# Optimization experiments

Hardware: AMD Instinct MI355X
Metric: run time of the kernel (lower is better)

Reference implementation:

```python
import jax, jax.numpy as jnp
import numpy as np

DIM = 1024
HEADS = 16
DIM_HEAD = 64
INNER = HEADS * DIM_HEAD  # == DIM, so project_out Linear is shape-consistent
SCALE = DIM_HEAD ** -0.5
EPS = 1e-5


def setup_inputs() -> dict:
    key = jax.random.key(0)
    ks = jax.random.split(key, 8)
    std = 0.02
    return {
        "x": jax.random.normal(ks[0], (2, 2048, DIM), dtype=jnp.float32),
        "gamma": jnp.ones((DIM,), dtype=jnp.float32),
        "beta": jnp.zeros((DIM,), dtype=jnp.float32),
        "wq": jax.random.normal(ks[1], (DIM, INNER), dtype=jnp.float32) * std,
        "wk": jax.random.normal(ks[2], (DIM, INNER), dtype=jnp.float32) * std,
        "wv": jax.random.normal(ks[3], (DIM, INNER), dtype=jnp.float32) * std,
        "wo": jax.random.normal(ks[4], (INNER, DIM), dtype=jnp.float32) * std,
        "w_out": jax.random.normal(ks[5], (INNER, DIM), dtype=jnp.float32) * std,
        "b_out": jnp.zeros((DIM,), dtype=jnp.float32),
    }


def reference(x, gamma, beta, wq, wk, wv, wo, w_out, b_out):
    b, n, d = x.shape
    # LayerNorm
    mu = jnp.mean(x, axis=-1, keepdims=True)
    var = jnp.mean(jnp.square(x - mu), axis=-1, keepdims=True)
    xn = (x - mu) * jax.lax.rsqrt(var + EPS) * gamma + beta
    # QKV projections -> [b, h, n, dh]
    def split_heads(t):
        return t.reshape(b, n, HEADS, DIM_HEAD).transpose(0, 2, 1, 3)
    q = split_heads(xn @ wq)
    k = split_heads(xn @ wk)
    v = split_heads(xn @ wv)
    scores = jnp.einsum('bhqd,bhkd->bhqk', q, k) * SCALE
    attn = jax.nn.softmax(scores, axis=-1)
    out = jnp.einsum('bhqk,bhkd->bhqd', attn, v)
    out = out.transpose(0, 2, 1, 3).reshape(b, n, INNER)
    out = out @ wo               # wo: inner -> dim
    out = out @ w_out + b_out    # project_out Linear (dropout=0 -> identity)
    return out
```

## Files before the change

kernel.cpp:

```cpp
#include <hip/hip_runtime.h>

typedef _Float16 f16;
typedef _Float16 f16x2 __attribute__((ext_vector_type(2)));
typedef _Float16 f16x4 __attribute__((ext_vector_type(4)));
typedef _Float16 f16x8 __attribute__((ext_vector_type(8)));
typedef float f32x4 __attribute__((ext_vector_type(4)));

#define MFMA_F16(a, b, c) __builtin_amdgcn_mfma_f32_16x16x32_f16(a, b, c, 0, 0, 0)
#define ASYNC16(g, l) __builtin_amdgcn_global_load_lds(                              \
    (const __attribute__((address_space(1))) void*)(g),                              \
    (__attribute__((address_space(3))) void*)(l), 16, 0, 0)

__global__ __launch_bounds__(256)
void pre_kernel(const float* __restrict__ x, const float* __restrict__ gamma,
                const float* __restrict__ beta, f16* __restrict__ xn,
                const float* __restrict__ wq, const float* __restrict__ wk,
                const float* __restrict__ wv, const float* __restrict__ wo,
                const float* __restrict__ wout,
                f16* __restrict__ wqt, f16* __restrict__ wkt, f16* __restrict__ wvt,
                f16* __restrict__ wo_h, f16* __restrict__ woutt)
{
    const int t = threadIdx.x;
    if (blockIdx.x < 4096) {
        const int row = blockIdx.x;
        const float* xr = x + (size_t)row * 1024;
        float4 v = *(const float4*)(xr + t * 4);
        float s  = v.x + v.y + v.z + v.w;
        float ss = v.x * v.x + v.y * v.y + v.z * v.z + v.w * v.w;
#pragma unroll
        for (int off = 32; off > 0; off >>= 1) {
            s  += __shfl_down(s, off);
            ss += __shfl_down(ss, off);
        }
        __shared__ float wsum[4], wsq[4];
        const int wid = t >> 6, lane = t & 63;
        if (lane == 0) { wsum[wid] = s; wsq[wid] = ss; }
        __syncthreads();
        const float fs  = wsum[0] + wsum[1] + wsum[2] + wsum[3];
        const float fss = wsq[0] + wsq[1] + wsq[2] + wsq[3];
        const float mu  = fs * (1.0f / 1024.0f);
        const float var = fss * (1.0f / 1024.0f) - mu * mu;
        const float rs  = rsqrtf(var + 1e-5f);
        float4 g = *(const float4*)(gamma + t * 4);
        float4 b = *(const float4*)(beta + t * 4);
        f16x4 o;
        o[0] = (f16)((v.x - mu) * rs * g.x + b.x);
        o[1] = (f16)((v.y - mu) * rs * g.y + b.y);
        o[2] = (f16)((v.z - mu) * rs * g.z + b.z);
        o[3] = (f16)((v.w - mu) * rs * g.w + b.w);
        *(f16x4*)(xn + (size_t)row * 1024 + t * 4) = o;
        return;
    }
    const int pb = blockIdx.x - 4096;
    const int z = pb >> 8, rem = pb & 255;
    const int bx = rem & 15, by = rem >> 4;
    const float* src; f16* dst; int tr; float scl = 1.0f;
    switch (z) {
        case 0:  src = wq;   dst = wqt;   tr = 1; scl = 0.18033688011f; break;
        case 1:  src = wk;   dst = wkt;   tr = 1; break;
        case 2:  src = wv;   dst = wvt;   tr = 1; break;
        case 3:  src = wo;   dst = wo_h;  tr = 0; break;
        default: src = wout; dst = woutt; tr = 1; break;
    }
    const int r0 = by * 64, c0 = bx * 64;
    if (!tr) {
#pragma unroll
        for (int i = 0; i < 16; i++) {
            int idx = t + 256 * i;
            int r = idx >> 6, c = idx & 63;
            dst[(size_t)(r0 + r) * 1024 + c0 + c] = (f16)src[(size_t)(r0 + r) * 1024 + c0 + c];
        }
    } else {
        __shared__ __align__(16) f16 T[64][72];
#pragma unroll
        for (int i = 0; i < 16; i++) {
            int idx = t + 256 * i;
            int r = idx >> 6, c = idx & 63;
            T[r][c] = (f16)(src[(size_t)(r0 + r) * 1024 + c0 + c] * scl);
        }
        __syncthreads();
#pragma unroll
        for (int i = 0; i < 16; i++) {
            int idx = t + 256 * i;
            int r = idx >> 6, c = idx & 63;
            dst[(size_t)(c0 + r) * 1024 + r0 + c] = T[c][r];
        }
    }
}

__global__ __launch_bounds__(256, 3)
void gemm_qkv_w2(const f16* __restrict__ A, const f16* __restrict__ Bt,
                 f16* __restrict__ Qd, f16* __restrict__ Kd, f16* __restrict__ Vd,
                 const f16* __restrict__ A2, const f16* __restrict__ Bt2,
                 f16* __restrict__ W2t)
{
    __shared__ __align__(16) f16 smem[2 * 128 * 64];
    f16* As = smem;
    f16* Bs = smem + 128 * 64;
    const int tid = threadIdx.x;
    const int wid = tid >> 6, lane = tid & 63;
    const int qq = lane >> 4, ml = lane & 15;
    const int row0 = (wid >> 1) * 64, col0 = (wid & 1) * 64;

    int mode, bx, by;
    const f16 *Abase, *Bbase;
    if (blockIdx.y < 24) {
        mode = 0; bx = blockIdx.x; by = blockIdx.y; Abase = A; Bbase = Bt;
    } else {
        mode = 1;
        int id = (blockIdx.y - 24) * 32 + blockIdx.x;
        bx = id & 7; by = id >> 3; Abase = A2; Bbase = Bt2;
    }
    const f16* Ab = Abase + (size_t)bx * 128 * 1024;
    const f16* Bb = Bbase + (size_t)by * 128 * 1024;
    const int sr = lane >> 3;
    const int sc = ((lane & 7) ^ sr) * 8;
    const int swz = ml & 7;

    f32x4 acc[4][4];
#pragma unroll
    for (int i = 0; i < 4; i++)
#pragma unroll
        for (int j = 0; j < 4; j++) acc[i][j] = (f32x4){0.f, 0.f, 0.f, 0.f};

    for (int k0 = 0; k0 < 1024; k0 += 64) {
        __syncthreads();
#pragma unroll
        for (int j = 0; j < 4; j++) {
            const int inst = wid * 4 + j;
            const int r = inst * 8 + sr;
            ASYNC16(Ab + (size_t)r * 1024 + k0 + sc, &As[inst * 512]);
            ASYNC16(Bb + (size_t)r * 1024 + k0 + sc, &Bs[inst * 512]);
        }
        __syncthreads();
#pragma unroll
        for (int kh = 0; kh < 2; kh++) {
            f16x8 af[4], bf[4];
#pragma unroll
            for (int mb = 0; mb < 4; mb++)
                af[mb] = *(const f16x8*)(&As[(row0 + mb * 16 + ml) * 64 + ((kh * 4 + qq) ^ swz) * 8]);
#pragma unroll
            for (int nb = 0; nb < 4; nb++)
                bf[nb] = *(const f16x8*)(&Bs[(col0 + nb * 16 + ml) * 64 + ((kh * 4 + qq) ^ swz) * 8]);
#pragma unroll
            for (int mb = 0; mb < 4; mb++)
#pragma unroll
                for (int nb = 0; nb < 4; nb++)
                    acc[mb][nb] = MFMA_F16(af[mb], bf[nb], acc[mb][nb]);
        }
    }

    if (mode == 1) {
        const int rT = bx * 128 + row0 + qq * 4;
#pragma unroll
        for (int mb = 0; mb < 4; mb++)
#pragma unroll
            for (int nb = 0; nb < 4; nb++) {
                int c = by * 128 + col0 + nb * 16 + ml;
#pragma unroll
                for (int rg = 0; rg < 4; rg++)
                    W2t[(size_t)(rT + mb * 16 + rg) * 1024 + c] = (f16)acc[mb][nb][rg];
            }
        return;
    }
    __syncthreads();
    f16* Cs = smem;
    const int sel = (by * 128) >> 10;
    const int bb  = (bx * 128) >> 11;
    const int nl0 = (bx * 128) & 2047;
    const int h0  = (by & 7) * 2;
    if (sel < 2) {
#pragma unroll
        for (int mb = 0; mb < 4; mb++)
#pragma unroll
            for (int nb = 0; nb < 4; nb++) {
                int col = col0 + nb * 16 + ml;
#pragma unroll
                for (int rg = 0; rg < 4; rg++) {
                    int row = row0 + mb * 16 + qq * 4 + rg;
                    int ch = (col >> 3) ^ (row & 15);
                    Cs[row * 128 + ch * 8 + (col & 7)] = (f16)acc[mb][nb][rg];
                }
            }
        __syncthreads();
        f16* Dst = (sel == 0 ? Qd : Kd);
#pragma unroll
        for (int i = 0; i < 8; i++) {
            int idx = i * 256 + tid;
            int r = idx >> 4, ch = idx & 15;
            f16x8 v = *(const f16x8*)(&Cs[r * 128 + ((ch ^ (r & 15)) * 8)]);
            int hh = h0 + (ch >> 3), d0 = (ch & 7) * 8;
            *(f16x8*)(Dst + ((size_t)(bb * 16 + hh) * 2048 + nl0 + r) * 64 + d0) = v;
        }
    } else {
#pragma unroll
        for (int mb = 0; mb < 4; mb++)
#pragma unroll
            for (int nb = 0; nb < 4; nb++) {
                int col = col0 + nb * 16 + ml;
                int rch = ((row0 + mb * 16) >> 3) + (qq >> 1);
                int ch = rch ^ (col & 15);
                f16x4 w;
                w[0] = (f16)acc[mb][nb][0]; w[1] = (f16)acc[mb][nb][1];
                w[2] = (f16)acc[mb][nb][2]; w[3] = (f16)acc[mb][nb][3];
                *(f16x4*)(&Cs[col * 128 + ch * 8 + (qq & 1) * 4]) = w;
            }
        __syncthreads();
#pragma unroll
        for (int i = 0; i < 8; i++) {
            int idx = i * 256 + tid;
            int c = idx >> 4, tc = idx & 15;
            f16x8 v = *(const f16x8*)(&Cs[c * 128 + ((tc ^ (c & 15)) * 8)]);
            int hh = h0 + (c >> 6), d = c & 63;
            *(f16x8*)(Vd + ((size_t)(bb * 16 + hh) * 64 + d) * 2048 + nl0 + tc * 8) = v;
        }
    }
}

__global__ __launch_bounds__(256, 4)
void flash_kernel(const f16* __restrict__ Q, const f16* __restrict__ K,
                  const f16* __restrict__ Vt, f16* __restrict__ O)
{
    __shared__ __align__(16) f16 Ks[2][64 * 64];
    __shared__ __align__(16) f16 Vts[2][64 * 64];
    __shared__ __align__(16) f16 Ps[4][16 * 64];

    const int bh = blockIdx.y;
    const int q0 = blockIdx.x * 64;
    const int tid = threadIdx.x, wid = tid >> 6, lane = tid & 63;
    const int qq = lane >> 4, ml = lane & 15;

    const f16* Qb = Q + ((size_t)bh * 2048 + q0 + wid * 16) * 64;
    const f16* Kb = K + (size_t)bh * 2048 * 64;
    const f16* Vb = Vt + (size_t)bh * 64 * 2048;

    f16x8 qf[2];
#pragma unroll
    for (int kh = 0; kh < 2; kh++)
        qf[kh] = *(const f16x8*)(Qb + (size_t)ml * 64 + kh * 32 + qq * 8);

    f32x4 oacc[4];
    float lsum = 0.f;
#pragma unroll
    for (int nd = 0; nd < 4; nd++) oacc[nd] = (f32x4){0.f, 0.f, 0.f, 0.f};

    const int sr = lane >> 3, scw = ((lane & 7) ^ sr) * 8;
    const int swz = ml & 7;
    f16* Psw = Ps[wid];

#pragma unroll
    for (int j = 0; j < 2; j++) {
        const int inst = wid * 2 + j;
        const int r = inst * 8 + sr;
        ASYNC16(Kb + (size_t)r * 64 + scw, &Ks[0][inst * 512]);
        ASYNC16(Vb + (size_t)r * 2048 + 0 + scw, &Vts[0][inst * 512]);
    }
    __syncthreads();

    for (int t = 0; t < 32; t++) {
        const int buf = t & 1;
        if (t < 31) {
            const int t1 = (t + 1) * 64;
#pragma unroll
            for (int j = 0; j < 2; j++) {
                const int inst = wid * 2 + j;
                const int r = inst * 8 + sr;
                ASYNC16(Kb + ((size_t)t1 + r) * 64 + scw, &Ks[buf ^ 1][inst * 512]);
                ASYNC16(Vb + (size_t)r * 2048 + t1 + scw, &Vts[buf ^ 1][inst * 512]);
            }
        }

        f32x4 s[4];
#pragma unroll
        for (int nb = 0; nb < 4; nb++) s[nb] = (f32x4){0.f, 0.f, 0.f, 0.f};
#pragma unroll
        for (int nb = 0; nb < 4; nb++)
#pragma unroll
            for (int kh = 0; kh < 2; kh++) {
                f16x8 kb = *(const f16x8*)(&Ks[buf][(nb * 16 + ml) * 64 + ((kh * 4 + qq) ^ swz) * 8]);
                s[nb] = MFMA_F16(kb, qf[kh], s[nb]);
            }

#pragma unroll
        for (int nb = 0; nb < 4; nb++) {
            float p0 = __builtin_amdgcn_exp2f(s[nb][0]);
            float p1 = __builtin_amdgcn_exp2f(s[nb][1]);
            float p2 = __builtin_amdgcn_exp2f(s[nb][2]);
            float p3 = __builtin_amdgcn_exp2f(s[nb][3]);
            lsum += (p0 + p1) + (p2 + p3);
            f16x2 lo = __builtin_bit_cast(f16x2, __builtin_amdgcn_cvt_pkrtz(p0, p1));
            f16x2 hi = __builtin_bit_cast(f16x2, __builtin_amdgcn_cvt_pkrtz(p2, p3));
            f16x4 w = __builtin_shufflevector(lo, hi, 0, 1, 2, 3);
            int ch = (2 * nb + (qq >> 1)) ^ swz;
            *(f16x4*)(&Psw[ml * 64 + ch * 8 + (qq & 1) * 4]) = w;
        }

#pragma unroll
        for (int ks = 0; ks < 2; ks++) {
            f16x8 pa = *(const f16x8*)(&Psw[ml * 64 + ((ks * 4 + 2 * (qq >> 1) + (qq & 1)) ^ swz) * 8]);
#pragma unroll
            for (int nd = 0; nd < 4; nd++) {
                f16x8 vb = *(const f16x8*)(&Vts[buf][(nd * 16 + ml) * 64 + ((ks * 4 + qq) ^ swz) * 8]);
                oacc[nd] = MFMA_F16(pa, vb, oacc[nd]);
            }
        }
        __syncthreads();
    }

    lsum += __shfl_xor(lsum, 16);
    lsum += __shfl_xor(lsum, 32);

    const int bb = bh >> 4, hh = bh & 15;
#pragma unroll
    for (int r = 0; r < 4; r++) {
        float linv = 1.0f / __shfl(lsum, qq * 4 + r, 16);
        int tok = q0 + wid * 16 + qq * 4 + r;
        size_t base = ((size_t)(bb * 2048 + tok)) * 1024 + hh * 64;
#pragma unroll
        for (int nd = 0; nd < 4; nd++)
            O[base + nd * 16 + ml] = (f16)(oacc[nd][r] * linv);
    }
}

__global__ __launch_bounds__(256, 3)
void gemm_final(const f16* __restrict__ A, const f16* __restrict__ Bt,
                float* __restrict__ C, const float* __restrict__ bias)
{
    __shared__ __align__(16) f16 smem[2 * 128 * 64];
    f16* As = smem;
    f16* Bs = smem + 128 * 64;
    const int tid = threadIdx.x;
    const int wid = tid >> 6, lane = tid & 63;
    const int qq = lane >> 4, ml = lane & 15;
    const int row0 = (wid >> 1) * 64, col0 = (wid & 1) * 64;
    const f16* Ab = A + (size_t)blockIdx.x * 128 * 1024;
    const f16* Bb = Bt + (size_t)blockIdx.y * 128 * 1024;
    const int sr = lane >> 3;
    const int sc = ((lane & 7) ^ sr) * 8;
    const int swz = ml & 7;

    f32x4 acc[4][4];
#pragma unroll
    for (int i = 0; i < 4; i++)
#pragma unroll
        for (int j = 0; j < 4; j++) acc[i][j] = (f32x4){0.f, 0.f, 0.f, 0.f};

    for (int k0 = 0; k0 < 1024; k0 += 64) {
        __syncthreads();
#pragma unroll
        for (int j = 0; j < 4; j++) {
            const int inst = wid * 4 + j;
            const int r = inst * 8 + sr;
            ASYNC16(Ab + (size_t)r * 1024 + k0 + sc, &As[inst * 512]);
            ASYNC16(Bb + (size_t)r * 1024 + k0 + sc, &Bs[inst * 512]);
        }
        __syncthreads();
#pragma unroll
        for (int kh = 0; kh < 2; kh++) {
            f16x8 af[4], bf[4];
#pragma unroll
            for (int mb = 0; mb < 4; mb++)
                af[mb] = *(const f16x8*)(&As[(row0 + mb * 16 + ml) * 64 + ((kh * 4 + qq) ^ swz) * 8]);
#pragma unroll
            for (int nb = 0; nb < 4; nb++)
                bf[nb] = *(const f16x8*)(&Bs[(col0 + nb * 16 + ml) * 64 + ((kh * 4 + qq) ^ swz) * 8]);
#pragma unroll
            for (int mb = 0; mb < 4; mb++)
#pragma unroll
                for (int nb = 0; nb < 4; nb++)
                    acc[mb][nb] = MFMA_F16(af[mb], bf[nb], acc[mb][nb]);
        }
    }

    const int rT = blockIdx.x * 128 + row0 + qq * 4;
#pragma unroll
    for (int mb = 0; mb < 4; mb++)
#pragma unroll
        for (int nb = 0; nb < 4; nb++) {
            int c = blockIdx.y * 128 + col0 + nb * 16 + ml;
            float bv = bias[c];
#pragma unroll
            for (int rg = 0; rg < 4; rg++)
                C[(size_t)(rT + mb * 16 + rg) * 1024 + c] = acc[mb][nb][rg] + bv;
        }
}

extern "C" void kernel_launch(void* const* d_in, const int* in_sizes, int n_in,
                              void* d_out, int out_size, void* d_ws, size_t ws_size,
                              hipStream_t stream)
{
    const float* x     = (const float*)d_in[0];
    const float* gamma = (const float*)d_in[1];
    const float* beta  = (const float*)d_in[2];
    const float* wq    = (const float*)d_in[3];
    const float* wk    = (const float*)d_in[4];
    const float* wv    = (const float*)d_in[5];
    const float* wo    = (const float*)d_in[6];
    const float* wout  = (const float*)d_in[7];
    const float* bout  = (const float*)d_in[8];
    float* out = (float*)d_out;

    char* ws = (char*)d_ws;
    const size_t MB = 1 << 20;
    f16* xn    = (f16*)(ws + 0);
    f16* wqt   = (f16*)(ws + 8 * MB);
    f16* wkt   = (f16*)(ws + 10 * MB);
    f16* wvt   = (f16*)(ws + 12 * MB);
    f16* wo_h  = (f16*)(ws + 14 * MB);
    f16* woutt = (f16*)(ws + 16 * MB);
    f16* W2t   = (f16*)(ws + 18 * MB);
    f16* Qh    = (f16*)(ws + 20 * MB);
    f16* Kh    = (f16*)(ws + 28 * MB);
    f16* Vth   = (f16*)(ws + 36 * MB);
    f16* Oh    = xn;

    pre_kernel<<<5376, 256, 0, stream>>>(x, gamma, beta, xn, wq, wk, wv, wo, wout,
                                         wqt, wkt, wvt, wo_h, woutt);
    gemm_qkv_w2<<<dim3(32, 26), 256, 0, stream>>>(xn, wqt, Qh, Kh, Vth,
                                                  woutt, wo_h, W2t);
    flash_kernel<<<dim3(32, 32), 256, 0, stream>>>(Qh, Kh, Vth, Oh);
    gemm_final<<<dim3(32, 8), 256, 0, stream>>>(Oh, W2t, out, bout);
}
```

Before: 208.8 us.

## Rewrite flash attention with 32x32 MFMA and register-resident P via lane shuffles

```diff
diff --git a/kernel.cpp b/kernel.cpp
--- a/kernel.cpp
+++ b/kernel.cpp
@@ -5,8 +5,10 @@
 typedef _Float16 f16x4 __attribute__((ext_vector_type(4)));
 typedef _Float16 f16x8 __attribute__((ext_vector_type(8)));
 typedef float f32x4 __attribute__((ext_vector_type(4)));
+typedef float f32x16 __attribute__((ext_vector_type(16)));
 
 #define MFMA_F16(a, b, c) __builtin_amdgcn_mfma_f32_16x16x32_f16(a, b, c, 0, 0, 0)
+#define MFMA32_F16(a, b, c) __builtin_amdgcn_mfma_f32_32x32x16_f16(a, b, c, 0, 0, 0)
 #define ASYNC16(g, l) __builtin_amdgcn_global_load_lds(                              \
     (const __attribute__((address_space(1))) void*)(g),                              \
     (__attribute__((address_space(3))) void*)(l), 16, 0, 0)
@@ -217,43 +219,44 @@
     }
 }
 
-__global__ __launch_bounds__(256, 4)
+__global__ __launch_bounds__(256, 2)
 void flash_kernel(const f16* __restrict__ Q, const f16* __restrict__ K,
                   const f16* __restrict__ Vt, f16* __restrict__ O)
 {
     __shared__ __align__(16) f16 Ks[2][64 * 64];
     __shared__ __align__(16) f16 Vts[2][64 * 64];
-    __shared__ __align__(16) f16 Ps[4][16 * 64];
 
     const int bh = blockIdx.y;
-    const int q0 = blockIdx.x * 64;
+    const int q0 = blockIdx.x * 128;
     const int tid = threadIdx.x, wid = tid >> 6, lane = tid & 63;
-    const int qq = lane >> 4, ml = lane & 15;
-
-    const f16* Qb = Q + ((size_t)bh * 2048 + q0 + wid * 16) * 64;
+    const int ql = lane & 31;
+    const int h  = lane >> 5;
+    const int sw = ql & 7;
+
+    const f16* Qb = Q + ((size_t)bh * 2048 + q0 + wid * 32) * 64;
     const f16* Kb = K + (size_t)bh * 2048 * 64;
     const f16* Vb = Vt + (size_t)bh * 64 * 2048;
 
-    f16x8 qf[2];
-#pragma unroll
-    for (int kh = 0; kh < 2; kh++)
-        qf[kh] = *(const f16x8*)(Qb + (size_t)ml * 64 + kh * 32 + qq * 8);
-
-    f32x4 oacc[4];
+    f16x8 qf[4];
+#pragma unroll
+    for (int kt = 0; kt < 4; kt++)
+        qf[kt] = *(const f16x8*)(Qb + (size_t)ql * 64 + kt * 16 + h * 8);
+
+    f32x16 oacc[2];
+#pragma unroll
+    for (int db = 0; db < 2; db++)
+#pragma unroll
+        for (int r = 0; r < 16; r++) oacc[db][r] = 0.f;
     float lsum = 0.f;
-#pragma unroll
-    for (int nd = 0; nd < 4; nd++) oacc[nd] = (f32x4){0.f, 0.f, 0.f, 0.f};
 
     const int sr = lane >> 3, scw = ((lane & 7) ^ sr) * 8;
-    const int swz = ml & 7;
-    f16* Psw = Ps[wid];
 
 #pragma unroll
     for (int j = 0; j < 2; j++) {
         const int inst = wid * 2 + j;
         const int r = inst * 8 + sr;
         ASYNC16(Kb + (size_t)r * 64 + scw, &Ks[0][inst * 512]);
-        ASYNC16(Vb + (size_t)r * 2048 + 0 + scw, &Vts[0][inst * 512]);
+        ASYNC16(Vb + (size_t)r * 2048 + scw, &Vts[0][inst * 512]);
     }
     __syncthreads();
 
@@ -270,56 +273,72 @@
             }
         }
 
-        f32x4 s[4];
-#pragma unroll
-        for (int nb = 0; nb < 4; nb++) s[nb] = (f32x4){0.f, 0.f, 0.f, 0.f};
-#pragma unroll
-        for (int nb = 0; nb < 4; nb++)
-#pragma unroll
-            for (int kh = 0; kh < 2; kh++) {
-                f16x8 kb = *(const f16x8*)(&Ks[buf][(nb * 16 + ml) * 64 + ((kh * 4 + qq) ^ swz) * 8]);
-                s[nb] = MFMA_F16(kb, qf[kh], s[nb]);
-            }
-
-#pragma unroll
-        for (int nb = 0; nb < 4; nb++) {
-            float p0 = __builtin_amdgcn_exp2f(s[nb][0]);
-            float p1 = __builtin_amdgcn_exp2f(s[nb][1]);
-            float p2 = __builtin_amdgcn_exp2f(s[nb][2]);
-            float p3 = __builtin_amdgcn_exp2f(s[nb][3]);
-            lsum += (p0 + p1) + (p2 + p3);
-            f16x2 lo = __builtin_bit_cast(f16x2, __builtin_amdgcn_cvt_pkrtz(p0, p1));
-            f16x2 hi = __builtin_bit_cast(f16x2, __builtin_amdgcn_cvt_pkrtz(p2, p3));
-            f16x4 w = __builtin_shufflevector(lo, hi, 0, 1, 2, 3);
-            int ch = (2 * nb + (qq >> 1)) ^ swz;
-            *(f16x4*)(&Psw[ml * 64 + ch * 8 + (qq & 1) * 4]) = w;
-        }
-
-#pragma unroll
-        for (int ks = 0; ks < 2; ks++) {
-            f16x8 pa = *(const f16x8*)(&Psw[ml * 64 + ((ks * 4 + 2 * (qq >> 1) + (qq & 1)) ^ swz) * 8]);
-#pragma unroll
-            for (int nd = 0; nd < 4; nd++) {
-                f16x8 vb = *(const f16x8*)(&Vts[buf][(nd * 16 + ml) * 64 + ((ks * 4 + qq) ^ swz) * 8]);
-                oacc[nd] = MFMA_F16(pa, vb, oacc[nd]);
-            }
-        }
-        __syncthreads();
-    }
-
-    lsum += __shfl_xor(lsum, 16);
-    lsum += __shfl_xor(lsum, 32);
+        f32x16 s0, s1;
+#pragma unroll
+        for (int r = 0; r < 16; r++) { s0[r] = 0.f; s1[r] = 0.f; }
+#pragma unroll
+        for (int kt = 0; kt < 4; kt++) {
+            const int ch = ((kt * 2 + h) ^ sw) * 8;
+            f16x8 kf0 = *(const f16x8*)(&Ks[buf][ql * 64 + ch]);
+            f16x8 kf1 = *(const f16x8*)(&Ks[buf][(32 + ql) * 64 + ch]);
+            s0 = MFMA32_F16(kf0, qf[kt], s0);
+            s1 = MFMA32_F16(kf1, qf[kt], s1);
+        }
+
+        f16x2 pk[2][8], xp[2][8];
+#pragma unroll
+        for (int i = 0; i < 8; i++) {
+            float a0 = __builtin_amdgcn_exp2f(s0[2 * i]);
+            float a1 = __builtin_amdgcn_exp2f(s0[2 * i + 1]);
+            float b0 = __builtin_amdgcn_exp2f(s1[2 * i]);
+            float b1 = __builtin_amdgcn_exp2f(s1[2 * i + 1]);
+            lsum += (a0 + a1) + (b0 + b1);
+            pk[0][i] = __builtin_bit_cast(f16x2, __builtin_amdgcn_cvt_pkrtz(a0, a1));
+            pk[1][i] = __builtin_bit_cast(f16x2, __builtin_amdgcn_cvt_pkrtz(b0, b1));
+        }
+#pragma unroll
+        for (int kb = 0; kb < 2; kb++)
+#pragma unroll
+            for (int i = 0; i < 8; i++)
+                xp[kb][i] = __builtin_bit_cast(f16x2,
+                    __shfl_xor(__builtin_bit_cast(int, pk[kb][i]), 32));
+
+#pragma unroll
+        for (int kt = 0; kt < 4; kt++) {
+            const int kb = kt >> 1, c = (kt & 1) * 4;
+            f16x2 b0 = h ? xp[kb][c + 2] : pk[kb][c];
+            f16x2 b1 = h ? xp[kb][c + 3] : pk[kb][c + 1];
+            f16x2 b2 = h ? pk[kb][c + 2] : xp[kb][c];
+            f16x2 b3 = h ? pk[kb][c + 3] : xp[kb][c + 1];
+            f16x8 pb;
+            pb[0] = b0[0]; pb[1] = b0[1]; pb[2] = b1[0]; pb[3] = b1[1];
+            pb[4] = b2[0]; pb[5] = b2[1]; pb[6] = b3[0]; pb[7] = b3[1];
+            const int ch = ((kt * 2 + h) ^ sw) * 8;
+            f16x8 vf0 = *(const f16x8*)(&Vts[buf][ql * 64 + ch]);
+            f16x8 vf1 = *(const f16x8*)(&Vts[buf][(32 + ql) * 64 + ch]);
+            oacc[0] = MFMA32_F16(vf0, pb, oacc[0]);
+            oacc[1] = MFMA32_F16(vf1, pb, oacc[1]);
+        }
+        __syncthreads();
+    }
+
+    lsum += __builtin_bit_cast(float, __shfl_xor(__builtin_bit_cast(int, lsum), 32));
+    const float linv = 1.0f / lsum;
 
     const int bb = bh >> 4, hh = bh & 15;
-#pragma unroll
-    for (int r = 0; r < 4; r++) {
-        float linv = 1.0f / __shfl(lsum, qq * 4 + r, 16);
-        int tok = q0 + wid * 16 + qq * 4 + r;
-        size_t base = ((size_t)(bb * 2048 + tok)) * 1024 + hh * 64;
-#pragma unroll
-        for (int nd = 0; nd < 4; nd++)
-            O[base + nd * 16 + ml] = (f16)(oacc[nd][r] * linv);
-    }
+    const int tok = q0 + wid * 32 + ql;
+    f16* Ob = O + ((size_t)(bb * 2048 + tok)) * 1024 + hh * 64 + 4 * h;
+#pragma unroll
+    for (int db = 0; db < 2; db++)
+#pragma unroll
+        for (int m = 0; m < 4; m++) {
+            f16x2 lo = __builtin_bit_cast(f16x2, __builtin_amdgcn_cvt_pkrtz(
+                oacc[db][4 * m] * linv, oacc[db][4 * m + 1] * linv));
+            f16x2 hi = __builtin_bit_cast(f16x2, __builtin_amdgcn_cvt_pkrtz(
+                oacc[db][4 * m + 2] * linv, oacc[db][4 * m + 3] * linv));
+            f16x4 w; w[0] = lo[0]; w[1] = lo[1]; w[2] = hi[0]; w[3] = hi[1];
+            *(f16x4*)(Ob + db * 32 + m * 8) = w;
+        }
 }
 
 __global__ __launch_bounds__(256, 3)
@@ -418,6 +437,6 @@
                                          wqt, wkt, wvt, wo_h, woutt);
     gemm_qkv_w2<<<dim3(32, 26), 256, 0, stream>>>(xn, wqt, Qh, Kh, Vth,
                                                   woutt, wo_h, W2t);
-    flash_kernel<<<dim3(32, 32), 256, 0, stream>>>(Qh, Kh, Vth, Oh);
+    flash_kernel<<<dim3(16, 32), 256, 0, stream>>>(Qh, Kh, Vth, Oh);
     gemm_final<<<dim3(32, 8), 256, 0, stream>>>(Oh, W2t, out, bout);
 }
```

Result: slower. 216.1 us (+3.5%).
